# Kernel tuning notes

Hardware: AMD Instinct MI355X
Metric: run time of the kernel (lower is better)

Reference implementation:

```python
import jax, jax.numpy as jnp
import numpy as np

B, N, S = 32, 4096, 11          # batch, n_inputs (64x64 feature map), n_slots
D_IN, D, MLP = 512, 512, 2048   # input feat dim, qkv_size, mlp hidden
ITERS = 3                       # num_iterations
EPS_ATTN = 1e-8                 # renormalize epsilon
EPS_LN = 1e-5                   # torch LayerNorm default eps


def layer_norm(x, g, b, eps=EPS_LN):
    mu = jnp.mean(x, axis=-1, keepdims=True)
    var = jnp.mean(jnp.square(x - mu), axis=-1, keepdims=True)
    return (x - mu) * jax.lax.rsqrt(var + eps) * g + b


def setup_inputs() -> dict:
    key = jax.random.key(0)
    ks = jax.random.split(key, 16)
    s = 0.02
    return {
        "slots": jax.random.normal(ks[0], (B, S, D), jnp.float32),
        "inputs": jax.random.normal(ks[1], (B, N, D_IN), jnp.float32),
        # input LayerNorm
        "ln_in_g": jnp.ones((D_IN,), jnp.float32),
        "ln_in_b": jnp.zeros((D_IN,), jnp.float32),
        # k / v projections (with bias, like nn.Linear)
        "Wk": jax.random.normal(ks[2], (D_IN, D), jnp.float32) * s,
        "bk": jnp.zeros((D,), jnp.float32),
        "Wv": jax.random.normal(ks[3], (D_IN, D), jnp.float32) * s,
        "bv": jnp.zeros((D,), jnp.float32),
        # query LayerNorm + bias-free q projection
        "ln_q_g": jnp.ones((D,), jnp.float32),
        "ln_q_b": jnp.zeros((D,), jnp.float32),
        "Wq": jax.random.normal(ks[4], (D, D), jnp.float32) * s,
        # GRUCell: gate order (r, z, n), torch layout [3D, D]
        "W_ih": jax.random.normal(ks[5], (3 * D, D), jnp.float32) * s,
        "b_ih": jnp.zeros((3 * D,), jnp.float32),
        "W_hh": jax.random.normal(ks[6], (3 * D, D), jnp.float32) * s,
        "b_hh": jnp.zeros((3 * D,), jnp.float32),
        # MLP: LN -> Linear -> ReLU -> Linear (no residual in source)
        "ln_m_g": jnp.ones((D,), jnp.float32),
        "ln_m_b": jnp.zeros((D,), jnp.float32),
        "W1": jax.random.normal(ks[7], (D, MLP), jnp.float32) * s,
        "b1": jnp.zeros((MLP,), jnp.float32),
        "W2": jax.random.normal(ks[8], (MLP, D), jnp.float32) * s,
        "b2": jnp.zeros((D,), jnp.float32),
    }


def reference(slots, inputs, ln_in_g, ln_in_b, Wk, bk, Wv, bv,
              ln_q_g, ln_q_b, Wq, W_ih, b_ih, W_hh, b_hh,
              ln_m_g, ln_m_b, W1, b1, W2, b2):
    # inputs LN + k/v projections (computed once, outside the loop)
    x = layer_norm(inputs, ln_in_g, ln_in_b)          # [B, N, D_IN]
    k = x @ Wk + bk                                   # [B, N, D]
    v = x @ Wv + bv                                   # [B, N, D]
    scale = 1.0 / jnp.sqrt(jnp.asarray(D, slots.dtype))

    for _ in range(ITERS):
        # q projection
        q = layer_norm(slots, ln_q_g, ln_q_b) @ Wq    # [B, S, D]
        # inverted attention: softmax over slot (query) axis
        logits = jnp.einsum('bsd,bnd->bsn', q * scale, k)  # [B, S, N]
        attn = jax.nn.softmax(logits, axis=-2)        # over S (inverted)
        # renormalize over keys (mean norm)
        attn = attn / (jnp.sum(attn, axis=-1, keepdims=True) + EPS_ATTN)
        updates = jnp.einsum('bsn,bnd->bsd', attn, v)  # [B, S, D]

        # GRUCell(updates, slots) -- torch semantics, gate order (r, z, n)
        gi = updates @ W_ih.T + b_ih                  # [B, S, 3D]
        gh = slots @ W_hh.T + b_hh                    # [B, S, 3D]
        ir, iz, in_ = jnp.split(gi, 3, axis=-1)
        hr, hz, hn = jnp.split(gh, 3, axis=-1)
        r = jax.nn.sigmoid(ir + hr)
        z = jax.nn.sigmoid(iz + hz)
        n = jnp.tanh(in_ + r * hn)
        slots = (1.0 - z) * n + z * slots

        # MLP (note: source assigns slots = mlp(slots), no residual)
        h = layer_norm(slots, ln_m_g, ln_m_b)
        slots = jax.nn.relu(h @ W1 + b1) @ W2 + b2
    return slots
```

## Files before the change

kernel.cpp:

```cpp
#include <hip/hip_runtime.h>
#include <cstdint>
#include <cstddef>

typedef short bf16x8 __attribute__((ext_vector_type(8)));
typedef float floatx4 __attribute__((ext_vector_type(4)));
typedef unsigned short ushort4v __attribute__((ext_vector_type(4)));

#define LN_EPS 1e-5f
#define ATTN_EPS 1e-8f
#define NCHUNK 16

__device__ __forceinline__ unsigned short f2bf(float f) {
    unsigned int u = __float_as_uint(f);
    u += 0x7fffu + ((u >> 16) & 1u);
    return (unsigned short)(u >> 16);
}

__device__ __forceinline__ void load_lds16(const void* gp, void* lp) {
    __builtin_amdgcn_global_load_lds(
        (__attribute__((address_space(1))) void*)gp,
        (__attribute__((address_space(3))) void*)lp,
        16, 0, 0);
}

template<bool OUT_BF16, bool QDOT>
__global__ __launch_bounds__(256) void ln512_kernel(
        const float* __restrict__ x, const float* __restrict__ g, const float* __restrict__ b,
        void* __restrict__ out, int total_rows, int data_rows, float outscale,
        const float* __restrict__ wqbk, float* __restrict__ cbuf) {
    int row = blockIdx.x * 4 + (threadIdx.x >> 6);
    int lane = threadIdx.x & 63;
    if (row >= total_rows) return;
    int rr = row < data_rows ? row : data_rows - 1;
    const float4* xr = (const float4*)(x + (size_t)rr * 512);
    float4 a0 = xr[lane];
    float4 a1 = xr[lane + 64];
    float s  = a0.x + a0.y + a0.z + a0.w + a1.x + a1.y + a1.z + a1.w;
    float ss = a0.x*a0.x + a0.y*a0.y + a0.z*a0.z + a0.w*a0.w
             + a1.x*a1.x + a1.y*a1.y + a1.z*a1.z + a1.w*a1.w;
    #pragma unroll
    for (int off = 32; off > 0; off >>= 1) {
        s  += __shfl_xor(s, off, 64);
        ss += __shfl_xor(ss, off, 64);
    }
    float mu = s * (1.0f / 512.0f);
    float var = ss * (1.0f / 512.0f) - mu * mu;
    float rstd = rsqrtf(var + LN_EPS);
    float4 g0 = ((const float4*)g)[lane];
    float4 g1 = ((const float4*)g)[lane + 64];
    float4 b0 = ((const float4*)b)[lane];
    float4 b1 = ((const float4*)b)[lane + 64];
    float y[8];
    y[0] = ((a0.x - mu) * rstd * g0.x + b0.x) * outscale;
    y[1] = ((a0.y - mu) * rstd * g0.y + b0.y) * outscale;
    y[2] = ((a0.z - mu) * rstd * g0.z + b0.z) * outscale;
    y[3] = ((a0.w - mu) * rstd * g0.w + b0.w) * outscale;
    y[4] = ((a1.x - mu) * rstd * g1.x + b1.x) * outscale;
    y[5] = ((a1.y - mu) * rstd * g1.y + b1.y) * outscale;
    y[6] = ((a1.z - mu) * rstd * g1.z + b1.z) * outscale;
    y[7] = ((a1.w - mu) * rstd * g1.w + b1.w) * outscale;
    if (QDOT) {
        float4 w0 = ((const float4*)wqbk)[lane];
        float4 w1 = ((const float4*)wqbk)[lane + 64];
        float cd = y[0]*w0.x + y[1]*w0.y + y[2]*w0.z + y[3]*w0.w
                 + y[4]*w1.x + y[5]*w1.y + y[6]*w1.z + y[7]*w1.w;
        #pragma unroll
        for (int off = 32; off > 0; off >>= 1) cd += __shfl_xor(cd, off, 64);
        if (lane == 0) cbuf[row] = cd;
    }
    if (OUT_BF16) {
        unsigned short* orow = (unsigned short*)out + (size_t)row * 512;
        ushort4v o0, o1;
        o0.x = f2bf(y[0]); o0.y = f2bf(y[1]); o0.z = f2bf(y[2]); o0.w = f2bf(y[3]);
        o1.x = f2bf(y[4]); o1.y = f2bf(y[5]); o1.z = f2bf(y[6]); o1.w = f2bf(y[7]);
        *(ushort4v*)(orow + lane * 4) = o0;
        *(ushort4v*)(orow + 256 + lane * 4) = o1;
    } else {
        float* orow = (float*)out + (size_t)row * 512;
        *(float4*)(orow + lane * 4) = make_float4(y[0], y[1], y[2], y[3]);
        *(float4*)(orow + 256 + lane * 4) = make_float4(y[4], y[5], y[6], y[7]);
    }
}

__device__ __forceinline__ void tr32(const float* __restrict__ in, unsigned short* __restrict__ out,
                                     int R, int C, int bx, int by, float (*tile)[33]) {
    int tx = threadIdx.x & 31, ty = threadIdx.x >> 5;
    #pragma unroll
    for (int i = 0; i < 32; i += 8)
        tile[ty + i][tx] = in[(size_t)(by + ty + i) * C + bx + tx];
    __syncthreads();
    #pragma unroll
    for (int i = 0; i < 32; i += 8)
        out[(size_t)(bx + ty + i) * R + by + tx] = f2bf(tile[tx][ty + i]);
}

__device__ __forceinline__ void rowdot512(const float* __restrict__ in, const float* __restrict__ vec,
                                          float* __restrict__ out, int row) {
    int lane = threadIdx.x & 63;
    const float4* r0 = (const float4*)(in + (size_t)row * 512);
    float4 a0 = r0[lane], a1 = r0[lane + 64];
    float4 v0 = ((const float4*)vec)[lane], v1 = ((const float4*)vec)[lane + 64];
    float d = a0.x*v0.x + a0.y*v0.y + a0.z*v0.z + a0.w*v0.w
            + a1.x*v1.x + a1.y*v1.y + a1.z*v1.z + a1.w*v1.w;
    #pragma unroll
    for (int off = 32; off > 0; off >>= 1) d += __shfl_xor(d, off, 64);
    if (lane == 0) out[row] = d;
}

__global__ __launch_bounds__(256) void prep_all(
        const float* __restrict__ Wk, const float* __restrict__ Wq,
        const float* __restrict__ Wv, const float* __restrict__ W_ih,
        const float* __restrict__ W_hh, const float* __restrict__ W1,
        const float* __restrict__ W2, const float* __restrict__ slots_in,
        const float* __restrict__ bk, const float* __restrict__ bv,
        unsigned short* __restrict__ Wk_b, unsigned short* __restrict__ Wq_b,
        unsigned short* __restrict__ Wv_b, unsigned short* __restrict__ Wih_b,
        unsigned short* __restrict__ Whh_b, unsigned short* __restrict__ W1T,
        unsigned short* __restrict__ W2T, unsigned short* __restrict__ slbf,
        float* __restrict__ wqbk, float* __restrict__ bvW, float* __restrict__ slots) {
    __shared__ float tile[32][33];
    const int b = blockIdx.x;
    const int t = threadIdx.x;
    if (b < 1024) {
        int idx = b * 256 + t; Wk_b[idx] = f2bf(Wk[idx]);
    } else if (b < 2048) {
        int idx = (b - 1024) * 256 + t; Wq_b[idx] = f2bf(Wq[idx]);
    } else if (b < 3072) {
        int idx = (b - 2048) * 256 + t; Wv_b[idx] = f2bf(Wv[idx]);
    } else if (b < 6144) {
        int idx = (b - 3072) * 256 + t; Wih_b[idx] = f2bf(W_ih[idx]);
    } else if (b < 9216) {
        int idx = (b - 6144) * 256 + t; Whh_b[idx] = f2bf(W_hh[idx]);
    } else if (b < 10240) {
        int i = b - 9216;
        tr32(W1, W1T, 512, 2048, (i & 63) * 32, (i >> 6) * 32, tile);
    } else if (b < 11264) {
        int i = b - 10240;
        tr32(W2, W2T, 2048, 512, (i & 15) * 32, (i >> 4) * 32, tile);
    } else if (b < 12032) {
        int idx = (b - 11264) * 256 + t;
        int row = idx >> 9, d = idx & 511;
        int rr = row < 352 ? row : 351;
        slbf[idx] = f2bf(slots_in[(size_t)rr * 512 + d]);
    } else if (b < 12160) {
        int row = (b - 12032) * 4 + (t >> 6);
        rowdot512(Wq, bk, wqbk, row);
    } else if (b < 12288) {
        int row = (b - 12160) * 4 + (t >> 6);
        rowdot512(W_ih, bv, bvW, row);
    } else {
        int idx = (b - 12288) * 256 + t;
        slots[idx] = slots_in[idx];
    }
}

template<int BMODE, bool RELU, int OUT_MODE>
__device__ __forceinline__ void hgemm_core(
        const unsigned short* __restrict__ A, const unsigned short* __restrict__ Bt,
        const float* __restrict__ bias, const float* __restrict__ bvW,
        const float* __restrict__ coef, float* __restrict__ Cf,
        unsigned short* __restrict__ Cb, int m0, int n0, int N, int K,
        unsigned short* As0, unsigned short* Bs0,
        unsigned short* As1, unsigned short* Bs1) {
    const int t = threadIdx.x;
    const int lane = t & 63;
    const int w = t >> 6;
    const int wm = w >> 1, wn = w & 1;
    const int quad = lane >> 4;
    const int l15 = lane & 15;
    floatx4 acc[2][2];
    #pragma unroll
    for (int i = 0; i < 2; ++i)
        #pragma unroll
        for (int j = 0; j < 2; ++j)
            #pragma unroll
            for (int r = 0; r < 4; ++r) acc[i][j][r] = 0.0f;

    auto stage = [&](unsigned short* Asd, unsigned short* Bsd, int k0) {
        #pragma unroll
        for (int p = 0; p < 2; ++p) {
            const int s = p * 256 + t;
            const int row = s >> 3;
            const int c = (s & 7) ^ (row & 7);
            const int ldsoff = (s - lane) * 16;
            load_lds16(A  + (size_t)(m0 + row) * K + k0 + c * 8, (char*)Asd + ldsoff);
            load_lds16(Bt + (size_t)(n0 + row) * K + k0 + c * 8, (char*)Bsd + ldsoff);
        }
    };
    auto compute = [&](const unsigned short* Asr, const unsigned short* Bsr) {
        #pragma unroll
        for (int h = 0; h < 2; ++h) {
            bf16x8 af[2], bfr[2];
            #pragma unroll
            for (int i = 0; i < 2; ++i) {
                const int row = wm * 32 + i * 16 + l15;
                const int cp = ((h << 2) | quad) ^ (l15 & 7);
                af[i] = *(const bf16x8*)(Asr + row * 64 + cp * 8);
            }
            #pragma unroll
            for (int j = 0; j < 2; ++j) {
                const int row = wn * 32 + j * 16 + l15;
                const int cp = ((h << 2) | quad) ^ (l15 & 7);
                bfr[j] = *(const bf16x8*)(Bsr + row * 64 + cp * 8);
            }
            #pragma unroll
            for (int i = 0; i < 2; ++i)
                #pragma unroll
                for (int j = 0; j < 2; ++j)
                    acc[i][j] = __builtin_amdgcn_mfma_f32_16x16x32_bf16(af[i], bfr[j], acc[i][j], 0, 0, 0);
        }
    };

    const int nk = K >> 6;
    stage(As0, Bs0, 0);
    for (int ki = 0; ki < nk; ++ki) {
        const bool odd = (ki & 1) != 0;
        unsigned short* Ac = odd ? As1 : As0;
        unsigned short* Bc = odd ? Bs1 : Bs0;
        if (ki + 1 < nk) {
            stage(odd ? As0 : As1, odd ? Bs0 : Bs1, (ki + 1) * 64);
            asm volatile("s_waitcnt vmcnt(4)" ::: "memory");
        } else {
            asm volatile("s_waitcnt vmcnt(0)" ::: "memory");
        }
        __builtin_amdgcn_s_barrier();
        __builtin_amdgcn_sched_barrier(0);
        compute(Ac, Bc);
        __builtin_amdgcn_sched_barrier(0);
        __builtin_amdgcn_s_barrier();
    }

    #pragma unroll
    for (int j = 0; j < 2; ++j) {
        const int n = n0 + wn * 32 + j * 16 + l15;
        const float bb = (BMODE >= 1) ? bias[n] : 0.0f;
        const float bw = (BMODE == 2) ? bvW[n] : 0.0f;
        #pragma unroll
        for (int i = 0; i < 2; ++i) {
            #pragma unroll
            for (int r = 0; r < 4; ++r) {
                const int m = m0 + wm * 32 + i * 16 + quad * 4 + r;
                float v = acc[i][j][r] + bb;
                if (BMODE == 2) v += coef[m] * bw;
                if (RELU) v = fmaxf(v, 0.0f);
                if (OUT_MODE == 0 || OUT_MODE == 2) Cf[(size_t)m * N + n] = v;
                if (OUT_MODE == 1 || OUT_MODE == 2) Cb[(size_t)m * N + n] = f2bf(v);
            }
        }
    }
}

template<int BMODE, bool RELU, int OUT_MODE>
__global__ __launch_bounds__(256) void hgemm(
        const unsigned short* __restrict__ A, const unsigned short* __restrict__ Bt,
        const float* __restrict__ bias, float* __restrict__ Cf,
        unsigned short* __restrict__ Cb, int N, int K) {
    __shared__ unsigned short As0[64 * 64];
    __shared__ unsigned short Bs0[64 * 64];
    __shared__ unsigned short As1[64 * 64];
    __shared__ unsigned short Bs1[64 * 64];
    hgemm_core<BMODE, RELU, OUT_MODE>(A, Bt, bias, nullptr, nullptr, Cf, Cb,
                                      blockIdx.y * 64, blockIdx.x * 64, N, K,
                                      As0, Bs0, As1, Bs1);
}

__global__ __launch_bounds__(256) void prep_gemms(
        const unsigned short* __restrict__ Wk_b, const unsigned short* __restrict__ Wq_b,
        const unsigned short* __restrict__ Wih_b, const unsigned short* __restrict__ Wv_b,
        unsigned short* __restrict__ WqkT, unsigned short* __restrict__ Wc) {
    __shared__ unsigned short As0[64 * 64];
    __shared__ unsigned short Bs0[64 * 64];
    __shared__ unsigned short As1[64 * 64];
    __shared__ unsigned short Bs1[64 * 64];
    if (blockIdx.z == 0) {
        if (blockIdx.y >= 8) return;
        hgemm_core<0, false, 1>(Wk_b, Wq_b, nullptr, nullptr, nullptr, nullptr, WqkT,
                                blockIdx.y * 64, blockIdx.x * 64, 512, 512,
                                As0, Bs0, As1, Bs1);
    } else {
        hgemm_core<0, false, 1>(Wih_b, Wv_b, nullptr, nullptr, nullptr, nullptr, Wc,
                                blockIdx.y * 64, blockIdx.x * 64, 512, 512,
                                As0, Bs0, As1, Bs1);
    }
}

__global__ __launch_bounds__(256) void gru_gemm(
        const unsigned short* __restrict__ Pn, const unsigned short* __restrict__ slbf,
        const unsigned short* __restrict__ Wc, const unsigned short* __restrict__ Whh,
        const float* __restrict__ bih, const float* __restrict__ bhh,
        const float* __restrict__ bvW, const float* __restrict__ coef,
        float* __restrict__ gi, float* __restrict__ gh) {
    __shared__ unsigned short As0[64 * 64];
    __shared__ unsigned short Bs0[64 * 64];
    __shared__ unsigned short As1[64 * 64];
    __shared__ unsigned short Bs1[64 * 64];
    if (blockIdx.z == 0)
        hgemm_core<2, false, 0>(Pn, Wc, bih, bvW, coef, gi, nullptr,
                                blockIdx.y * 64, blockIdx.x * 64, 1536, 512,
                                As0, Bs0, As1, Bs1);
    else
        hgemm_core<1, false, 0>(slbf, Whh, bhh, nullptr, nullptr, gh, nullptr,
                                blockIdx.y * 64, blockIdx.x * 64, 1536, 512,
                                As0, Bs0, As1, Bs1);
}

template<bool LN1>
__global__ __launch_bounds__(256, 2) void attn_kernel(
        const unsigned short* __restrict__ qp_b, unsigned short* xln,
        const float* __restrict__ cbuf,
        float* __restrict__ Up, float* __restrict__ rsp,
        const float* __restrict__ inputs,
        const float* __restrict__ ln_in_g, const float* __restrict__ ln_in_b) {
    const int b = blockIdx.y;
    const int chunk = blockIdx.x;
    const int w = threadIdx.x >> 6, lane = threadIdx.x & 63;
    const int l15 = lane & 15, quad = lane >> 4;
    const int d0 = lane * 8;
    const int NPC = 4096 / NCHUNK;

    __shared__ float Us[11 * 512];
    __shared__ float attnlds[64 * 20];
    __shared__ float rss[11];

    const size_t rowbase = (size_t)b * 4096 + (size_t)chunk * NPC;

    if (LN1) {
        float4 g0 = ((const float4*)ln_in_g)[lane];
        float4 g1 = ((const float4*)ln_in_g)[lane + 64];
        float4 b0 = ((const float4*)ln_in_b)[lane];
        float4 b1 = ((const float4*)ln_in_b)[lane + 64];
        for (int r = w; r < NPC; r += 4) {
            const float4* xr = (const float4*)(inputs + (rowbase + r) * 512);
            float4 a0 = xr[lane];
            float4 a1 = xr[lane + 64];
            float s  = a0.x + a0.y + a0.z + a0.w + a1.x + a1.y + a1.z + a1.w;
            float ss = a0.x*a0.x + a0.y*a0.y + a0.z*a0.z + a0.w*a0.w
                     + a1.x*a1.x + a1.y*a1.y + a1.z*a1.z + a1.w*a1.w;
            #pragma unroll
            for (int off = 32; off > 0; off >>= 1) {
                s  += __shfl_xor(s, off, 64);
                ss += __shfl_xor(ss, off, 64);
            }
            float mu = s * (1.0f / 512.0f);
            float var = ss * (1.0f / 512.0f) - mu * mu;
            float rstd = rsqrtf(var + LN_EPS);
            unsigned short* orow = xln + (rowbase + r) * 512;
            ushort4v o0, o1;
            o0.x = f2bf((a0.x - mu) * rstd * g0.x + b0.x);
            o0.y = f2bf((a0.y - mu) * rstd * g0.y + b0.y);
            o0.z = f2bf((a0.z - mu) * rstd * g0.z + b0.z);
            o0.w = f2bf((a0.w - mu) * rstd * g0.w + b0.w);
            o1.x = f2bf((a1.x - mu) * rstd * g1.x + b1.x);
            o1.y = f2bf((a1.y - mu) * rstd * g1.y + b1.y);
            o1.z = f2bf((a1.z - mu) * rstd * g1.z + b1.z);
            o1.w = f2bf((a1.w - mu) * rstd * g1.w + b1.w);
            *(ushort4v*)(orow + lane * 4) = o0;
            *(ushort4v*)(orow + 256 + lane * 4) = o1;
        }
        __syncthreads();
    }

    const unsigned short* qrow = qp_b + (size_t)(b * 11 + (l15 < 11 ? l15 : 10)) * 512 + quad * 8;
    bf16x8 aq[16];
    #pragma unroll
    for (int ks = 0; ks < 16; ++ks) aq[ks] = *(const bf16x8*)(qrow + ks * 32);

    float cb[4];
    #pragma unroll
    for (int r = 0; r < 4; ++r) {
        int s = quad * 4 + r;
        cb[r] = (s < 11) ? cbuf[b * 11 + s] : 0.0f;
    }

    float U[11][8];
    float rs[11];
    #pragma unroll
    for (int s = 0; s < 11; ++s) {
        rs[s] = 0.f;
        #pragma unroll
        for (int j = 0; j < 8; ++j) U[s][j] = 0.f;
    }

    const unsigned short* xbase = xln + rowbase * 512;

    for (int t = 0; t < NPC / 64; ++t) {
        const int n0 = t * 64 + w * 16;
        const unsigned short* krow = xbase + (size_t)(n0 + l15) * 512 + quad * 8;
        floatx4 c;
        c[0] = c[1] = c[2] = c[3] = 0.0f;
        #pragma unroll
        for (int ks = 0; ks < 16; ++ks) {
            bf16x8 bf = *(const bf16x8*)(krow + ks * 32);
            c = __builtin_amdgcn_mfma_f32_16x16x32_bf16(aq[ks], bf, c, 0, 0, 0);
        }
        float l0 = c[0] + cb[0], l1 = c[1] + cb[1], l2 = c[2] + cb[2], l3 = c[3] + cb[3];
        if (quad == 2) l3 = -1e30f;
        if (quad == 3) { l0 = -1e30f; l1 = -1e30f; l2 = -1e30f; l3 = -1e30f; }
        float mx = fmaxf(fmaxf(l0, l1), fmaxf(l2, l3));
        mx = fmaxf(mx, __shfl_xor(mx, 16, 64));
        mx = fmaxf(mx, __shfl_xor(mx, 32, 64));
        float e0 = __expf(l0 - mx), e1 = __expf(l1 - mx),
              e2 = __expf(l2 - mx), e3 = __expf(l3 - mx);
        float se = e0 + e1 + e2 + e3;
        se += __shfl_xor(se, 16, 64);
        se += __shfl_xor(se, 32, 64);
        float inv = 1.0f / se;
        float4 av = make_float4(e0 * inv, e1 * inv, e2 * inv, e3 * inv);
        *(float4*)&attnlds[(w * 16 + l15) * 20 + quad * 4] = av;
        __builtin_amdgcn_wave_barrier();
        for (int nl = 0; nl < 16; ++nl) {
            uint4 kr = *(const uint4*)(xbase + (size_t)(n0 + nl) * 512 + d0);
            float kf[8];
            kf[0] = __uint_as_float(kr.x << 16); kf[1] = __uint_as_float(kr.x & 0xffff0000u);
            kf[2] = __uint_as_float(kr.y << 16); kf[3] = __uint_as_float(kr.y & 0xffff0000u);
            kf[4] = __uint_as_float(kr.z << 16); kf[5] = __uint_as_float(kr.z & 0xffff0000u);
            kf[6] = __uint_as_float(kr.w << 16); kf[7] = __uint_as_float(kr.w & 0xffff0000u);
            const float* arow = &attnlds[(w * 16 + nl) * 20];
            float4 a0 = *(const float4*)(arow);
            float4 a1 = *(const float4*)(arow + 4);
            float4 a2 = *(const float4*)(arow + 8);
            float as[11] = {a0.x, a0.y, a0.z, a0.w, a1.x, a1.y, a1.z, a1.w,
                            a2.x, a2.y, a2.z};
            #pragma unroll
            for (int s = 0; s < 11; ++s) {
                rs[s] += as[s];
                #pragma unroll
                for (int j = 0; j < 8; ++j) U[s][j] = fmaf(as[s], kf[j], U[s][j]);
            }
        }
    }

    for (int ph = 0; ph < 4; ++ph) {
        if (w == ph) {
            #pragma unroll
            for (int s = 0; s < 11; ++s) {
                #pragma unroll
                for (int j = 0; j < 8; ++j) {
                    if (ph == 0) Us[s * 512 + d0 + j] = U[s][j];
                    else         Us[s * 512 + d0 + j] += U[s][j];
                }
            }
            if (lane == 0) {
                #pragma unroll
                for (int s = 0; s < 11; ++s) {
                    if (ph == 0) rss[s] = rs[s]; else rss[s] += rs[s];
                }
            }
        }
        __syncthreads();
    }
    float* up = Up + ((size_t)b * NCHUNK + chunk) * 11 * 512;
    for (int idx = threadIdx.x; idx < 11 * 512; idx += 256) up[idx] = Us[idx];
    if (threadIdx.x < 11) rsp[((size_t)b * NCHUNK + chunk) * 11 + threadIdx.x] = rss[threadIdx.x];
}

__global__ __launch_bounds__(256) void attn_reduce(
        const float* __restrict__ Up, const float* __restrict__ rsp,
        unsigned short* __restrict__ Pn, float* __restrict__ coef) {
    const int bs = blockIdx.x;
    if (bs >= 352) {
        for (int d = threadIdx.x; d < 512; d += 256) Pn[(size_t)bs * 512 + d] = 0;
        if (threadIdx.x == 0) coef[bs] = 0.0f;
        return;
    }
    const int b = bs / 11, s = bs - b * 11;
    float rsum = 0.0f;
    #pragma unroll
    for (int c = 0; c < NCHUNK; ++c) rsum += rsp[((size_t)b * NCHUNK + c) * 11 + s];
    const float inv = 1.0f / (rsum + ATTN_EPS);
    if (threadIdx.x == 0) coef[bs] = rsum * inv;
    for (int d = threadIdx.x; d < 512; d += 256) {
        float acc = 0.f;
        #pragma unroll
        for (int c = 0; c < NCHUNK; ++c) acc += Up[(((size_t)b * NCHUNK + c) * 11 + s) * 512 + d];
        Pn[(size_t)bs * 512 + d] = f2bf(acc * inv);
    }
}

__global__ __launch_bounds__(256) void gru_ln(
        const float* __restrict__ gi, const float* __restrict__ gh,
        const float* __restrict__ slots, const float* __restrict__ g,
        const float* __restrict__ b, unsigned short* __restrict__ mln) {
    int row = blockIdx.x * 4 + (threadIdx.x >> 6);
    int lane = threadIdx.x & 63;
    unsigned short* orow = mln + (size_t)row * 512;
    if (row >= 352) {
        ushort4v z; z.x = z.y = z.z = z.w = 0;
        *(ushort4v*)(orow + lane * 4) = z;
        *(ushort4v*)(orow + 256 + lane * 4) = z;
        return;
    }
    const float4* gir = (const float4*)(gi + (size_t)row * 1536);
    const float4* ghr = (const float4*)(gh + (size_t)row * 1536);
    const float4* sr  = (const float4*)(slots + (size_t)row * 512);
    float v[8];
    #pragma unroll
    for (int half = 0; half < 2; ++half) {
        int o = half * 64 + lane;
        float4 ir = gir[o], iz = gir[128 + o], in_ = gir[256 + o];
        float4 hr = ghr[o], hz = ghr[128 + o], hn = ghr[256 + o];
        float4 sv = sr[o];
        float rr[4], zz[4], nn[4];
        rr[0] = 1.f / (1.f + __expf(-(ir.x + hr.x)));
        rr[1] = 1.f / (1.f + __expf(-(ir.y + hr.y)));
        rr[2] = 1.f / (1.f + __expf(-(ir.z + hr.z)));
        rr[3] = 1.f / (1.f + __expf(-(ir.w + hr.w)));
        zz[0] = 1.f / (1.f + __expf(-(iz.x + hz.x)));
        zz[1] = 1.f / (1.f + __expf(-(iz.y + hz.y)));
        zz[2] = 1.f / (1.f + __expf(-(iz.z + hz.z)));
        zz[3] = 1.f / (1.f + __expf(-(iz.w + hz.w)));
        nn[0] = tanhf(in_.x + rr[0] * hn.x);
        nn[1] = tanhf(in_.y + rr[1] * hn.y);
        nn[2] = tanhf(in_.z + rr[2] * hn.z);
        nn[3] = tanhf(in_.w + rr[3] * hn.w);
        v[half * 4 + 0] = (1.f - zz[0]) * nn[0] + zz[0] * sv.x;
        v[half * 4 + 1] = (1.f - zz[1]) * nn[1] + zz[1] * sv.y;
        v[half * 4 + 2] = (1.f - zz[2]) * nn[2] + zz[2] * sv.z;
        v[half * 4 + 3] = (1.f - zz[3]) * nn[3] + zz[3] * sv.w;
    }
    float s = 0.f, ss = 0.f;
    #pragma unroll
    for (int j = 0; j < 8; ++j) { s += v[j]; ss += v[j] * v[j]; }
    #pragma unroll
    for (int off = 32; off > 0; off >>= 1) {
        s  += __shfl_xor(s, off, 64);
        ss += __shfl_xor(ss, off, 64);
    }
    float mu = s * (1.0f / 512.0f);
    float var = ss * (1.0f / 512.0f) - mu * mu;
    float rstd = rsqrtf(var + LN_EPS);
    float4 g0 = ((const float4*)g)[lane], g1 = ((const float4*)g)[lane + 64];
    float4 b0 = ((const float4*)b)[lane], b1 = ((const float4*)b)[lane + 64];
    ushort4v o0, o1;
    o0.x = f2bf((v[0] - mu) * rstd * g0.x + b0.x);
    o0.y = f2bf((v[1] - mu) * rstd * g0.y + b0.y);
    o0.z = f2bf((v[2] - mu) * rstd * g0.z + b0.z);
    o0.w = f2bf((v[3] - mu) * rstd * g0.w + b0.w);
    o1.x = f2bf((v[4] - mu) * rstd * g1.x + b1.x);
    o1.y = f2bf((v[5] - mu) * rstd * g1.y + b1.y);
    o1.z = f2bf((v[6] - mu) * rstd * g1.z + b1.z);
    o1.w = f2bf((v[7] - mu) * rstd * g1.w + b1.w);
    *(ushort4v*)(orow + lane * 4) = o0;
    *(ushort4v*)(orow + 256 + lane * 4) = o1;
}

extern "C" void kernel_launch(void* const* d_in, const int* in_sizes, int n_in,
                              void* d_out, int out_size, void* d_ws, size_t ws_size,
                              hipStream_t stream) {
    const float* slots_in = (const float*)d_in[0];
    const float* inputs   = (const float*)d_in[1];
    const float* ln_in_g  = (const float*)d_in[2];
    const float* ln_in_b  = (const float*)d_in[3];
    const float* Wk  = (const float*)d_in[4];
    const float* bk  = (const float*)d_in[5];
    const float* Wv  = (const float*)d_in[6];
    const float* bv  = (const float*)d_in[7];
    const float* ln_q_g = (const float*)d_in[8];
    const float* ln_q_b = (const float*)d_in[9];
    const float* Wq  = (const float*)d_in[10];
    const float* W_ih = (const float*)d_in[11];
    const float* b_ih = (const float*)d_in[12];
    const float* W_hh = (const float*)d_in[13];
    const float* b_hh = (const float*)d_in[14];
    const float* ln_m_g = (const float*)d_in[15];
    const float* ln_m_b = (const float*)d_in[16];
    const float* W1 = (const float*)d_in[17];
    const float* b1 = (const float*)d_in[18];
    const float* W2 = (const float*)d_in[19];
    const float* b2 = (const float*)d_in[20];

    char* p = (char*)d_ws;
    auto alloc = [&](size_t bytes) { char* r = p; p += (bytes + 255) & ~(size_t)255; return r; };
    unsigned short* xln   = (unsigned short*)alloc(131072ull * 512 * 2);
    unsigned short* Wk_b  = (unsigned short*)alloc(512ull * 512 * 2);
    unsigned short* Wq_b  = (unsigned short*)alloc(512ull * 512 * 2);
    unsigned short* Wv_b  = (unsigned short*)alloc(512ull * 512 * 2);
    unsigned short* Wih_b = (unsigned short*)alloc(1536ull * 512 * 2);
    unsigned short* Whh_b = (unsigned short*)alloc(1536ull * 512 * 2);
    unsigned short* WqkT  = (unsigned short*)alloc(512ull * 512 * 2);
    unsigned short* Wc    = (unsigned short*)alloc(1536ull * 512 * 2);
    unsigned short* W1T   = (unsigned short*)alloc(2048ull * 512 * 2);
    unsigned short* W2T   = (unsigned short*)alloc(512ull * 2048 * 2);
    unsigned short* slq   = (unsigned short*)alloc(384ull * 512 * 2);
    unsigned short* mln   = (unsigned short*)alloc(384ull * 512 * 2);
    unsigned short* Pn    = (unsigned short*)alloc(384ull * 512 * 2);
    unsigned short* slbf  = (unsigned short*)alloc(384ull * 512 * 2);
    unsigned short* h1    = (unsigned short*)alloc(384ull * 2048 * 2);
    unsigned short* qp_b  = (unsigned short*)alloc(384ull * 512 * 2);
    float* slots = (float*)alloc(384ull * 512 * 4);
    float* gi    = (float*)alloc(384ull * 1536 * 4);
    float* gh    = (float*)alloc(384ull * 1536 * 4);
    float* Up    = (float*)alloc((size_t)32 * NCHUNK * 11 * 512 * 4);
    float* rsp   = (float*)alloc((size_t)32 * NCHUNK * 11 * 4);
    float* wqbk  = (float*)alloc(512 * 4);
    float* bvW   = (float*)alloc(1536 * 4);
    float* cbuf  = (float*)alloc(384 * 4);
    float* coef  = (float*)alloc(384 * 4);

    prep_all<<<dim3(12992), 256, 0, stream>>>(
        Wk, Wq, Wv, W_ih, W_hh, W1, W2, slots_in, bk, bv,
        Wk_b, Wq_b, Wv_b, Wih_b, Whh_b, W1T, W2T, slbf, wqbk, bvW, slots);
    prep_gemms<<<dim3(8, 24, 2), 256, 0, stream>>>(Wk_b, Wq_b, Wih_b, Wv_b, WqkT, Wc);

    const float qscale = 0.044194173824159216f;
    for (int it = 0; it < 3; ++it) {
        ln512_kernel<true, true><<<dim3(96), 256, 0, stream>>>(
            slots, ln_q_g, ln_q_b, slq, 384, 352, qscale, wqbk, cbuf);
        hgemm<0, false, 1><<<dim3(8, 6), 256, 0, stream>>>(slq, WqkT, nullptr, nullptr, qp_b, 512, 512);
        if (it == 0)
            attn_kernel<true><<<dim3(NCHUNK, 32), 256, 0, stream>>>(
                qp_b, xln, cbuf, Up, rsp, inputs, ln_in_g, ln_in_b);
        else
            attn_kernel<false><<<dim3(NCHUNK, 32), 256, 0, stream>>>(
                qp_b, xln, cbuf, Up, rsp, nullptr, nullptr, nullptr);
        attn_reduce<<<dim3(384), 256, 0, stream>>>(Up, rsp, Pn, coef);
        gru_gemm<<<dim3(24, 6, 2), 256, 0, stream>>>(Pn, slbf, Wc, Whh_b, b_ih, b_hh, bvW, coef, gi, gh);
        gru_ln<<<dim3(96), 256, 0, stream>>>(gi, gh, slots, ln_m_g, ln_m_b, mln);
        hgemm<1, true, 1><<<dim3(32, 6), 256, 0, stream>>>(mln, W1T, b1, nullptr, h1, 2048, 512);
        hgemm<1, false, 2><<<dim3(8, 6), 256, 0, stream>>>(h1, W2T, b2, slots, slbf, 512, 2048);
    }
    hipMemcpyAsync(d_out, slots, (size_t)out_size * 4, hipMemcpyDeviceToDevice, stream);
}
```

Measured before the change: 749.6 us.

## Split attention-value accumulation across waves by feature columns instead of rows

Measured after the change: 843.3 us. 1.13x slower.

```diff
diff --git a/kernel.cpp b/kernel.cpp
--- a/kernel.cpp
+++ b/kernel.cpp
@@ -305,7 +305,7 @@
 }
 
 template<bool LN1>
-__global__ __launch_bounds__(256, 2) void attn_kernel(
+__global__ __launch_bounds__(256, 3) void attn_kernel(
         const unsigned short* __restrict__ qp_b, unsigned short* xln,
         const float* __restrict__ cbuf,
         float* __restrict__ Up, float* __restrict__ rsp,
@@ -315,14 +315,14 @@
     const int chunk = blockIdx.x;
     const int w = threadIdx.x >> 6, lane = threadIdx.x & 63;
     const int l15 = lane & 15, quad = lane >> 4;
-    const int d0 = lane * 8;
     const int NPC = 4096 / NCHUNK;
 
-    __shared__ float Us[11 * 512];
-    __shared__ float attnlds[64 * 20];
-    __shared__ float rss[11];
+    __shared__ float P[64][20];
+    __shared__ float rss[16];
 
     const size_t rowbase = (size_t)b * 4096 + (size_t)chunk * NPC;
+
+    if (threadIdx.x < 16) rss[threadIdx.x] = 0.0f;
 
     if (LN1) {
         float4 g0 = ((const float4*)ln_in_g)[lane];
@@ -372,28 +372,32 @@
         cb[r] = (s < 11) ? cbuf[b * 11 + s] : 0.0f;
     }
 
-    float U[11][8];
-    float rs[11];
-    #pragma unroll
-    for (int s = 0; s < 11; ++s) {
-        rs[s] = 0.f;
-        #pragma unroll
-        for (int j = 0; j < 8; ++j) U[s][j] = 0.f;
-    }
+    float U[11][2];
+    #pragma unroll
+    for (int s = 0; s < 11; ++s) { U[s][0] = 0.f; U[s][1] = 0.f; }
+    float4 rsacc = make_float4(0.f, 0.f, 0.f, 0.f);
 
     const unsigned short* xbase = xln + rowbase * 512;
+    const int d0 = w * 128 + lane * 2;
 
     for (int t = 0; t < NPC / 64; ++t) {
         const int n0 = t * 64 + w * 16;
         const unsigned short* krow = xbase + (size_t)(n0 + l15) * 512 + quad * 8;
-        floatx4 c;
-        c[0] = c[1] = c[2] = c[3] = 0.0f;
-        #pragma unroll
-        for (int ks = 0; ks < 16; ++ks) {
+        floatx4 ca, cb2;
+        ca[0] = ca[1] = ca[2] = ca[3] = 0.0f;
+        cb2[0] = cb2[1] = cb2[2] = cb2[3] = 0.0f;
+        #pragma unroll
+        for (int ks = 0; ks < 8; ++ks) {
             bf16x8 bf = *(const bf16x8*)(krow + ks * 32);
-            c = __builtin_amdgcn_mfma_f32_16x16x32_bf16(aq[ks], bf, c, 0, 0, 0);
-        }
-        float l0 = c[0] + cb[0], l1 = c[1] + cb[1], l2 = c[2] + cb[2], l3 = c[3] + cb[3];
+            ca = __builtin_amdgcn_mfma_f32_16x16x32_bf16(aq[ks], bf, ca, 0, 0, 0);
+        }
+        #pragma unroll
+        for (int ks = 8; ks < 16; ++ks) {
+            bf16x8 bf = *(const bf16x8*)(krow + ks * 32);
+            cb2 = __builtin_amdgcn_mfma_f32_16x16x32_bf16(aq[ks], bf, cb2, 0, 0, 0);
+        }
+        float l0 = ca[0] + cb2[0] + cb[0], l1 = ca[1] + cb2[1] + cb[1];
+        float l2 = ca[2] + cb2[2] + cb[2], l3 = ca[3] + cb2[3] + cb[3];
         if (quad == 2) l3 = -1e30f;
         if (quad == 3) { l0 = -1e30f; l1 = -1e30f; l2 = -1e30f; l3 = -1e30f; }
         float mx = fmaxf(fmaxf(l0, l1), fmaxf(l2, l3));
@@ -406,51 +410,50 @@
         se += __shfl_xor(se, 32, 64);
         float inv = 1.0f / se;
         float4 av = make_float4(e0 * inv, e1 * inv, e2 * inv, e3 * inv);
-        *(float4*)&attnlds[(w * 16 + l15) * 20 + quad * 4] = av;
-        __builtin_amdgcn_wave_barrier();
-        for (int nl = 0; nl < 16; ++nl) {
-            uint4 kr = *(const uint4*)(xbase + (size_t)(n0 + nl) * 512 + d0);
-            float kf[8];
-            kf[0] = __uint_as_float(kr.x << 16); kf[1] = __uint_as_float(kr.x & 0xffff0000u);
-            kf[2] = __uint_as_float(kr.y << 16); kf[3] = __uint_as_float(kr.y & 0xffff0000u);
-            kf[4] = __uint_as_float(kr.z << 16); kf[5] = __uint_as_float(kr.z & 0xffff0000u);
-            kf[6] = __uint_as_float(kr.w << 16); kf[7] = __uint_as_float(kr.w & 0xffff0000u);
-            const float* arow = &attnlds[(w * 16 + nl) * 20];
-            float4 a0 = *(const float4*)(arow);
-            float4 a1 = *(const float4*)(arow + 4);
-            float4 a2 = *(const float4*)(arow + 8);
-            float as[11] = {a0.x, a0.y, a0.z, a0.w, a1.x, a1.y, a1.z, a1.w,
-                            a2.x, a2.y, a2.z};
+        *(float4*)&P[w * 16 + l15][quad * 4] = av;
+        float4 rv = av;
+        #pragma unroll
+        for (int off = 1; off < 16; off <<= 1) {
+            rv.x += __shfl_xor(rv.x, off, 64);
+            rv.y += __shfl_xor(rv.y, off, 64);
+            rv.z += __shfl_xor(rv.z, off, 64);
+            rv.w += __shfl_xor(rv.w, off, 64);
+        }
+        rsacc.x += rv.x; rsacc.y += rv.y; rsacc.z += rv.z; rsacc.w += rv.w;
+        __syncthreads();
+
+        const unsigned short* arow = xbase + (size_t)(t * 64) * 512 + d0;
+        #pragma unroll 4
+        for (int nl = 0; nl < 64; ++nl) {
+            unsigned int kr = *(const unsigned int*)(arow + (size_t)nl * 512);
+            float klo = __uint_as_float(kr << 16);
+            float khi = __uint_as_float(kr & 0xffff0000u);
+            const float* pr = &P[nl][0];
+            float4 p0 = *(const float4*)(pr);
+            float4 p1 = *(const float4*)(pr + 4);
+            float4 p2 = *(const float4*)(pr + 8);
+            float as[11] = {p0.x, p0.y, p0.z, p0.w, p1.x, p1.y, p1.z, p1.w,
+                            p2.x, p2.y, p2.z};
             #pragma unroll
             for (int s = 0; s < 11; ++s) {
-                rs[s] += as[s];
-                #pragma unroll
-                for (int j = 0; j < 8; ++j) U[s][j] = fmaf(as[s], kf[j], U[s][j]);
+                U[s][0] = fmaf(as[s], klo, U[s][0]);
+                U[s][1] = fmaf(as[s], khi, U[s][1]);
             }
         }
-    }
-
-    for (int ph = 0; ph < 4; ++ph) {
-        if (w == ph) {
-            #pragma unroll
-            for (int s = 0; s < 11; ++s) {
-                #pragma unroll
-                for (int j = 0; j < 8; ++j) {
-                    if (ph == 0) Us[s * 512 + d0 + j] = U[s][j];
-                    else         Us[s * 512 + d0 + j] += U[s][j];
-                }
-            }
-            if (lane == 0) {
-                #pragma unroll
-                for (int s = 0; s < 11; ++s) {
-                    if (ph == 0) rss[s] = rs[s]; else rss[s] += rs[s];
-                }
-            }
-        }
         __syncthreads();
     }
+
     float* up = Up + ((size_t)b * NCHUNK + chunk) * 11 * 512;
-    for (int idx = threadIdx.x; idx < 11 * 512; idx += 256) up[idx] = Us[idx];
+    #pragma unroll
+    for (int s = 0; s < 11; ++s)
+        *(float2*)(up + s * 512 + d0) = make_float2(U[s][0], U[s][1]);
+    if (l15 == 0) {
+        atomicAdd(&rss[quad * 4 + 0], rsacc.x);
+        atomicAdd(&rss[quad * 4 + 1], rsacc.y);
+        atomicAdd(&rss[quad * 4 + 2], rsacc.z);
+        atomicAdd(&rss[quad * 4 + 3], rsacc.w);
+    }
+    __syncthreads();
     if (threadIdx.x < 11) rsp[((size_t)b * NCHUNK + chunk) * 11 + threadIdx.x] = rss[threadIdx.x];
 }
 
```
